# Optimization experiments

Measured on AMD Instinct MI355X. Metric: run time of the kernel, lower is better.

The kernel has to match this reference:

```python
import jax, jax.numpy as jnp
import numpy as np


def setup_inputs() -> dict:
    key = jax.random.key(0)
    k_x, k_pos, k_val, k_temp = jax.random.split(key, 4)
    B, T, D, N = 8, 2048, 512, 4096
    x = jax.random.normal(k_x, (B, T, D), dtype=jnp.float32)
    # module init: positions ~ N(0,1)*0.5, values ~ N(0,1)*0.02
    positions = jax.random.normal(k_pos, (N, D), dtype=jnp.float32) * 0.5
    values = jax.random.normal(k_val, (N, D), dtype=jnp.float32) * 0.02
    # 'trained' temperatures ~ U[4,6] so the RBF kernel does not underflow at D=512
    temperature = 4.0 + 2.0 * jax.random.uniform(k_temp, (N,), dtype=jnp.float32)
    # neuron_scale buffer at late-tide level (MAX_SCALE = 0.8)
    neuron_scale = jnp.full((N,), 0.8, dtype=jnp.float32)
    return {"x": x, "positions": positions, "values": values,
            "temperature": temperature, "neuron_scale": neuron_scale}


def reference(x, positions, values, temperature, neuron_scale):
    B, T, D = x.shape
    x_flat = x.reshape(-1, D)                                  # [M, D], M = B*T
    x_sq = jnp.sum(x_flat * x_flat, axis=-1, keepdims=True)    # [M, 1]
    p_sq = jnp.sum(positions * positions, axis=-1)             # [N]
    cross = x_flat @ positions.T                               # [M, N] GEMM
    dists = jnp.sqrt(jnp.maximum(x_sq + p_sq[None, :] - 2.0 * cross, 0.0))
    effective_temp = (jnp.abs(temperature) + 0.1) * neuron_scale  # [N]
    weights = jnp.exp(-dists / effective_temp[None, :])        # [M, N]
    weights = weights / (jnp.sum(weights, axis=-1, keepdims=True) + 1e-8)
    out = weights @ values                                     # [M, D] GEMM
    return out.reshape(B, T, D)
```

## Files before the change

### kernel.cpp

```cpp
#include <hip/hip_runtime.h>
#include <hip/hip_bf16.h>

typedef __attribute__((ext_vector_type(8))) short short8;
typedef __attribute__((ext_vector_type(4))) float f32x4;
typedef __attribute__((ext_vector_type(4))) unsigned short u16x4;

__device__ __forceinline__ unsigned short f2bf(float f) {
  union { float f; unsigned u; } v; v.f = f;
  unsigned r = v.u + 0x7fffu + ((v.u >> 16) & 1u);
  return (unsigned short)(r >> 16);
}

template <int EPI>
__global__ __launch_bounds__(512, 4) void rbf_gemm(
    const unsigned short* __restrict__ A, const unsigned short* __restrict__ Bt,
    int Ncols, int K,
    const float* __restrict__ xsq, const float* __restrict__ psq,
    const float* __restrict__ rtemp, unsigned short* __restrict__ Wout,
    float* __restrict__ part, int Mtot, const float* __restrict__ denin,
    float* __restrict__ outp, int row0, int ldOut) {
  constexpr int HALF = 16384;
  __shared__ __align__(16) unsigned short smem[2 * HALF];

  const int t = threadIdx.x;
  const int lane = t & 63, wid = t >> 6;
  const int wr = wid >> 1, wc = wid & 1;
  const int lr = lane & 15, lg = lane >> 4;

  const int nb = Ncols >> 7;
  const int nwg = gridDim.x;
  int swz = blockIdx.x;
  if ((nwg & 7) == 0) {
    int cpx = nwg >> 3;
    swz = (swz & 7) * cpx + (swz >> 3);
  }
  const int bm = swz / nb, bn = swz - bm * nb;

  const unsigned short* Ab = A + (size_t)bm * 128 * K;
  const unsigned short* Bb = Bt + (size_t)bn * 128 * K;

  const unsigned short* gA[2];
  const unsigned short* gB[2];
#pragma unroll
  for (int i = 0; i < 2; ++i) {
    const int idx = i * 512 + t;
    const int r = idx >> 3, c = idx & 7;
    const int cs = c ^ (r & 7);
    gA[i] = Ab + (size_t)r * K + cs * 8;
    gB[i] = Bb + (size_t)r * K + cs * 8;
  }
  const int dbase = wid << 9;

  int offA[2][2], offB[4][2];
#pragma unroll
  for (int mi = 0; mi < 2; ++mi) {
    const int ar = wr * 32 + mi * 16 + lr;
#pragma unroll
    for (int ks = 0; ks < 2; ++ks)
      offA[mi][ks] = ar * 64 + (((ks << 2) | lg) ^ (ar & 7)) * 8;
  }
#pragma unroll
  for (int ni = 0; ni < 4; ++ni) {
    const int br = wc * 64 + ni * 16 + lr;
#pragma unroll
    for (int ks = 0; ks < 2; ++ks)
      offB[ni][ks] = 8192 + br * 64 + (((ks << 2) | lg) ^ (br & 7)) * 8;
  }

  f32x4 acc[2][4];
#pragma unroll
  for (int i = 0; i < 2; ++i)
#pragma unroll
    for (int j = 0; j < 4; ++j) acc[i][j] = (f32x4){0.f, 0.f, 0.f, 0.f};

#define STAGE(koff, boff)                                                            \
  do {                                                                               \
    _Pragma("unroll")                                                                \
    for (int i = 0; i < 2; ++i) {                                                    \
      __builtin_amdgcn_global_load_lds(                                              \
          (const __attribute__((address_space(1))) void*)(gA[i] + (koff)),           \
          (__attribute__((address_space(3))) void*)(smem + (boff) + i * 4096 + dbase), \
          16, 0, 0);                                                                 \
      __builtin_amdgcn_global_load_lds(                                              \
          (const __attribute__((address_space(1))) void*)(gB[i] + (koff)),           \
          (__attribute__((address_space(3))) void*)(smem + (boff) + 8192 + i * 4096 + dbase), \
          16, 0, 0);                                                                 \
    }                                                                                \
  } while (0)

  STAGE(0, 0);
  __syncthreads();
  unsigned boff = 0;
  const int nsteps = K >> 6;
  for (int s = 0; s < nsteps; ++s) {
    if (s + 1 < nsteps) STAGE((s + 1) << 6, boff ^ HALF);
    const unsigned short* sb = smem + boff;
    short8 af[2][2], bf[4][2];
#pragma unroll
    for (int mi = 0; mi < 2; ++mi)
#pragma unroll
      for (int ks = 0; ks < 2; ++ks) af[mi][ks] = *(const short8*)&sb[offA[mi][ks]];
#pragma unroll
    for (int ni = 0; ni < 4; ++ni)
#pragma unroll
      for (int ks = 0; ks < 2; ++ks) bf[ni][ks] = *(const short8*)&sb[offB[ni][ks]];
#pragma unroll
    for (int ks = 0; ks < 2; ++ks)
#pragma unroll
      for (int mi = 0; mi < 2; ++mi)
#pragma unroll
        for (int ni = 0; ni < 4; ++ni)
          acc[mi][ni] = __builtin_amdgcn_mfma_f32_16x16x32_bf16(af[mi][ks], bf[ni][ks],
                                                                acc[mi][ni], 0, 0, 0);
    __syncthreads();
    boff ^= HALF;
  }
#undef STAGE

  if (EPI == 0) {
    float xv[2][4];
#pragma unroll
    for (int mi = 0; mi < 2; ++mi)
#pragma unroll
      for (int j = 0; j < 4; ++j)
        xv[mi][j] = xsq[row0 + bm * 128 + wr * 32 + mi * 16 + lg * 4 + j];

    float rs[2][4];
#pragma unroll
    for (int mi = 0; mi < 2; ++mi)
#pragma unroll
      for (int j = 0; j < 4; ++j) rs[mi][j] = 0.f;

#pragma unroll
    for (int ni = 0; ni < 4; ++ni) {
      const int lcol = wc * 64 + ni * 16 + lr;
      const int col = bn * 128 + lcol;
      const float ps = psq[col];
      const float rt = rtemp[col];
      const int h = lcol >> 3;
#pragma unroll
      for (int mi = 0; mi < 2; ++mi) {
#pragma unroll
        for (int j = 0; j < 4; ++j) {
          const int lrow = wr * 32 + mi * 16 + lg * 4 + j;
          float d2 = xv[mi][j] + ps - 2.0f * acc[mi][ni][j];
          float dist = __builtin_amdgcn_sqrtf(fmaxf(d2, 0.0f));
          float wgt = __expf(-dist * rt);
          smem[lrow * 128 + ((h ^ (lrow & 15)) << 3) + (lcol & 7)] = f2bf(wgt);
          rs[mi][j] += wgt;
        }
      }
    }
    __syncthreads();
#pragma unroll
    for (int i = 0; i < 4; ++i) {
      const int id = i * 512 + t;
      const int r = id >> 4, h = id & 15;
      short8 v = *(const short8*)&smem[r * 128 + ((h ^ (r & 15)) << 3)];
      __builtin_nontemporal_store(v,
          (short8*)&Wout[(size_t)(bm * 128 + r) * ldOut + bn * 128 + h * 8]);
    }
    float* slice = part + (size_t)((bn << 1) | wc) * Mtot;
#pragma unroll
    for (int mi = 0; mi < 2; ++mi)
#pragma unroll
      for (int j = 0; j < 4; ++j) {
        float v = rs[mi][j];
        v += __shfl_xor(v, 1);
        v += __shfl_xor(v, 2);
        v += __shfl_xor(v, 4);
        v += __shfl_xor(v, 8);
        if (lr == 0) {
          const int grow = row0 + bm * 128 + wr * 32 + mi * 16 + lg * 4 + j;
          __builtin_nontemporal_store(v, &slice[grow]);
        }
      }
  } else {
#pragma unroll
    for (int mi = 0; mi < 2; ++mi) {
#pragma unroll
      for (int j = 0; j < 4; ++j) {
        const int grow = row0 + bm * 128 + wr * 32 + mi * 16 + lg * 4 + j;
        const float rd = 1.0f / (denin[grow] + 1e-8f);
#pragma unroll
        for (int ni = 0; ni < 4; ++ni) {
          const int col = bn * 128 + wc * 64 + ni * 16 + lr;
          __builtin_nontemporal_store(acc[mi][ni][j] * rd,
                                      &outp[(size_t)grow * ldOut + col]);
        }
      }
    }
  }
}

__global__ void reduce_denom(const float* __restrict__ part, float* __restrict__ denom,
                             int Mtot, int row0, int S) {
  const int m = row0 + blockIdx.x * 128 + threadIdx.x;
  float s = 0.f;
  for (int i = 0; i < S; ++i) s += part[(size_t)i * Mtot + m];
  denom[m] = s;
}

__global__ void prep_rows(const float* __restrict__ in, unsigned short* __restrict__ outb,
                          float* __restrict__ sq, int D) {
  const int row = blockIdx.x;
  const int t = threadIdx.x;
  const float4 v = ((const float4*)(in + (size_t)row * D))[t];
  u16x4 o = {f2bf(v.x), f2bf(v.y), f2bf(v.z), f2bf(v.w)};
  *(u16x4*)(outb + (size_t)row * D + t * 4) = o;
  float s = v.x * v.x + v.y * v.y + v.z * v.z + v.w * v.w;
  for (int off = 32; off; off >>= 1) s += __shfl_xor(s, off);
  __shared__ float ws[16];
  if ((t & 63) == 0) ws[t >> 6] = s;
  __syncthreads();
  if (t == 0) {
    float tot = 0.f;
    const int nw = blockDim.x >> 6;
    for (int i = 0; i < nw; ++i) tot += ws[i];
    sq[row] = tot;
  }
}

__global__ void prep_scale(const float* __restrict__ tmp, const float* __restrict__ sc,
                           float* __restrict__ rtemp, int N) {
  const int i = blockIdx.x * blockDim.x + threadIdx.x;
  if (i < N) rtemp[i] = 1.0f / ((fabsf(tmp[i]) + 0.1f) * sc[i]);
}

__global__ void prep_vT(const float* __restrict__ vals, unsigned short* __restrict__ vT,
                        int N, int D) {
  __shared__ float tile[32][33];
  const int nt = blockIdx.x, dt = blockIdx.y;
  const int tx = threadIdx.x, ty = threadIdx.y;
#pragma unroll
  for (int i = 0; i < 4; ++i) {
    int r = nt * 32 + ty + i * 8;
    tile[ty + i * 8][tx] = vals[(size_t)r * D + dt * 32 + tx];
  }
  __syncthreads();
#pragma unroll
  for (int i = 0; i < 4; ++i) {
    int d = dt * 32 + ty + i * 8;
    vT[(size_t)d * N + nt * 32 + tx] = f2bf(tile[tx][ty + i * 8]);
  }
}

extern "C" void kernel_launch(void* const* d_in, const int* in_sizes, int n_in,
                              void* d_out, int out_size, void* d_ws, size_t ws_size,
                              hipStream_t stream) {
  const float* x = (const float*)d_in[0];
  const float* pos = (const float*)d_in[1];
  const float* vals = (const float*)d_in[2];
  const float* temp = (const float*)d_in[3];
  const float* nsc = (const float*)d_in[4];
  float* out = (float*)d_out;

  const int N = in_sizes[3];
  const int D = in_sizes[1] / N;
  const int M = in_sizes[0] / D;
  const int S = 2 * (N / 128);

  char* ws = (char*)d_ws;
  size_t off = 0;
  auto alloc = [&](size_t bytes) {
    void* p = ws + off;
    off = (off + bytes + 255) & ~(size_t)255;
    return p;
  };
  unsigned short* xb = (unsigned short*)alloc((size_t)M * D * 2);
  unsigned short* pb = (unsigned short*)alloc((size_t)N * D * 2);
  unsigned short* vT = (unsigned short*)alloc((size_t)D * N * 2);
  float* xsq = (float*)alloc((size_t)M * 4);
  float* psq = (float*)alloc((size_t)N * 4);
  float* rtemp = (float*)alloc((size_t)N * 4);
  float* denom = (float*)alloc((size_t)M * 4);
  float* part = (float*)alloc((size_t)S * M * 4);

  size_t avail = ws_size > off ? ws_size - off : 0;
  long long mc_ll = (long long)(avail / ((size_t)N * 2));
  int Mc = (int)((mc_ll / 128) * 128);
  if (Mc > M) Mc = M;
  if (Mc < 128) Mc = 128;
  unsigned short* W = (unsigned short*)alloc((size_t)Mc * N * 2);

  prep_rows<<<M, D / 4, 0, stream>>>(x, xb, xsq, D);
  prep_rows<<<N, D / 4, 0, stream>>>(pos, pb, psq, D);
  prep_scale<<<(N + 255) / 256, 256, 0, stream>>>(temp, nsc, rtemp, N);
  dim3 tg(N / 32, D / 32);
  prep_vT<<<tg, dim3(32, 8), 0, stream>>>(vals, vT, N, D);

  for (int row0 = 0; row0 < M; row0 += Mc) {
    const int mc = (M - row0) < Mc ? (M - row0) : Mc;
    const int g1 = (mc / 128) * (N / 128);
    rbf_gemm<0><<<g1, 512, 0, stream>>>(xb + (size_t)row0 * D, pb, N, D,
                                        xsq, psq, rtemp, W, part, M,
                                        nullptr, nullptr, row0, N);
    reduce_denom<<<mc / 128, 128, 0, stream>>>(part, denom, M, row0, S);
    const int g2 = (mc / 128) * (D / 128);
    rbf_gemm<1><<<g2, 512, 0, stream>>>(W, vT, D, N,
                                        nullptr, nullptr, nullptr, nullptr,
                                        part, M, denom, out, row0, D);
  }
}
```

Before: 230.0 us.

## Fuse distance GEMM, RBF weights and value GEMM into one flash-style kernel

```diff
diff --git a/kernel.cpp b/kernel.cpp
--- a/kernel.cpp
+++ b/kernel.cpp
@@ -11,203 +11,246 @@
   return (unsigned short)(r >> 16);
 }
 
-template <int EPI>
-__global__ __launch_bounds__(512, 4) void rbf_gemm(
-    const unsigned short* __restrict__ A, const unsigned short* __restrict__ Bt,
-    int Ncols, int K,
+#define GLL(src, dst)                                                     \
+  __builtin_amdgcn_global_load_lds(                                       \
+      (const __attribute__((address_space(1))) void*)(src),               \
+      (__attribute__((address_space(3))) void*)(dst), 16, 0, 0)
+#define BAR __builtin_amdgcn_s_barrier()
+
+__global__ __launch_bounds__(512, 2) void rbf_fused(
+    const unsigned short* __restrict__ xb, const unsigned short* __restrict__ pb,
+    const unsigned short* __restrict__ vT,
     const float* __restrict__ xsq, const float* __restrict__ psq,
-    const float* __restrict__ rtemp, unsigned short* __restrict__ Wout,
-    float* __restrict__ part, int Mtot, const float* __restrict__ denin,
-    float* __restrict__ outp, int row0, int ldOut) {
-  constexpr int HALF = 16384;
-  __shared__ __align__(16) unsigned short smem[2 * HALF];
-
+    const float* __restrict__ rtemp, float* __restrict__ out, int N, int Dk) {
+  __shared__ __align__(16) unsigned short smem[65536];
   const int t = threadIdx.x;
   const int lane = t & 63, wid = t >> 6;
-  const int wr = wid >> 1, wc = wid & 1;
   const int lr = lane & 15, lg = lane >> 4;
-
-  const int nb = Ncols >> 7;
-  const int nwg = gridDim.x;
-  int swz = blockIdx.x;
-  if ((nwg & 7) == 0) {
-    int cpx = nwg >> 3;
-    swz = (swz & 7) * cpx + (swz >> 3);
-  }
-  const int bm = swz / nb, bn = swz - bm * nb;
-
-  const unsigned short* Ab = A + (size_t)bm * 128 * K;
-  const unsigned short* Bb = Bt + (size_t)bn * 128 * K;
-
-  const unsigned short* gA[2];
-  const unsigned short* gB[2];
-#pragma unroll
-  for (int i = 0; i < 2; ++i) {
+  const int wm = wid >> 2, wn = wid & 3;
+  const int row0 = blockIdx.x * 64;
+
+  const unsigned short* Xb = xb + (size_t)row0 * Dk;
+
+#pragma unroll
+  for (int i = 0; i < 8; ++i) {
+    const int idx = i * 512 + t;
+    const int r = idx >> 6, c = idx & 63;
+    GLL(Xb + (size_t)r * Dk + ((c ^ (r & 7)) << 3), smem + i * 4096 + (wid << 9));
+  }
+  const unsigned short* gP[4];
+#pragma unroll
+  for (int i = 0; i < 4; ++i) {
     const int idx = i * 512 + t;
     const int r = idx >> 3, c = idx & 7;
-    const int cs = c ^ (r & 7);
-    gA[i] = Ab + (size_t)r * K + cs * 8;
-    gB[i] = Bb + (size_t)r * K + cs * 8;
-  }
-  const int dbase = wid << 9;
-
-  int offA[2][2], offB[4][2];
+    gP[i] = pb + (size_t)r * Dk + ((c ^ (r & 7)) << 3);
+  }
+
+#define STAGE_P(bufb, bump)                                               \
+  do {                                                                    \
+    _Pragma("unroll")                                                     \
+    for (int i = 0; i < 4; ++i) {                                         \
+      GLL(gP[i], smem + 32768 + (bufb) * 16384 + i * 4096 + (wid << 9));  \
+      gP[i] += (bump);                                                    \
+    }                                                                     \
+  } while (0)
+
+  STAGE_P(0, 64);
+
+  int offAx[2][2], offP[4][2], offW[4][2];
 #pragma unroll
   for (int mi = 0; mi < 2; ++mi) {
-    const int ar = wr * 32 + mi * 16 + lr;
+    const int ar = wm * 32 + mi * 16 + lr;
 #pragma unroll
     for (int ks = 0; ks < 2; ++ks)
-      offA[mi][ks] = ar * 64 + (((ks << 2) | lg) ^ (ar & 7)) * 8;
+      offAx[mi][ks] = ar * Dk + ((((ks << 2) | lg) ^ (ar & 7)) << 3);
   }
 #pragma unroll
   for (int ni = 0; ni < 4; ++ni) {
-    const int br = wc * 64 + ni * 16 + lr;
+    const int br = wn * 64 + ni * 16 + lr;
 #pragma unroll
     for (int ks = 0; ks < 2; ++ks)
-      offB[ni][ks] = 8192 + br * 64 + (((ks << 2) | lg) ^ (br & 7)) * 8;
-  }
-
-  f32x4 acc[2][4];
-#pragma unroll
-  for (int i = 0; i < 2; ++i)
-#pragma unroll
-    for (int j = 0; j < 4; ++j) acc[i][j] = (f32x4){0.f, 0.f, 0.f, 0.f};
-
-#define STAGE(koff, boff)                                                            \
-  do {                                                                               \
-    _Pragma("unroll")                                                                \
-    for (int i = 0; i < 2; ++i) {                                                    \
-      __builtin_amdgcn_global_load_lds(                                              \
-          (const __attribute__((address_space(1))) void*)(gA[i] + (koff)),           \
-          (__attribute__((address_space(3))) void*)(smem + (boff) + i * 4096 + dbase), \
-          16, 0, 0);                                                                 \
-      __builtin_amdgcn_global_load_lds(                                              \
-          (const __attribute__((address_space(1))) void*)(gB[i] + (koff)),           \
-          (__attribute__((address_space(3))) void*)(smem + (boff) + 8192 + i * 4096 + dbase), \
-          16, 0, 0);                                                                 \
-    }                                                                                \
-  } while (0)
-
-  STAGE(0, 0);
+      offP[ni][ks] = br * 64 + ((((ks << 2) | lg) ^ (br & 7)) << 3);
+  }
+#pragma unroll
+  for (int mi = 0; mi < 4; ++mi) {
+    const int ar = mi * 16 + lr;
+#pragma unroll
+    for (int ks = 0; ks < 2; ++ks)
+      offW[mi][ks] = 49152 + ar * 256 + ((((ks << 2) | lg) ^ (ar & 7)) << 3);
+  }
+  const unsigned short* vrow[4];
+#pragma unroll
+  for (int ni = 0; ni < 4; ++ni)
+    vrow[ni] = vT + (size_t)(wid * 64 + ni * 16 + lr) * N + lg * 8;
+
+  float xv[2][4];
+#pragma unroll
+  for (int mi = 0; mi < 2; ++mi)
+#pragma unroll
+    for (int j = 0; j < 4; ++j)
+      xv[mi][j] = xsq[row0 + wm * 32 + mi * 16 + lg * 4 + j];
+
+  f32x4 acc2[4][4];
+#pragma unroll
+  for (int i = 0; i < 4; ++i)
+#pragma unroll
+    for (int j = 0; j < 4; ++j) acc2[i][j] = (f32x4){0.f, 0.f, 0.f, 0.f};
+  float dreg[2][4];
+#pragma unroll
+  for (int mi = 0; mi < 2; ++mi)
+#pragma unroll
+    for (int j = 0; j < 4; ++j) dreg[mi][j] = 0.f;
+
+  const int nch = N >> 8;
+  const int nsl = nch * 8;
+  for (int nc = 0; nc < nch; ++nc) {
+    f32x4 acc1[2][4];
+#pragma unroll
+    for (int i = 0; i < 2; ++i)
+#pragma unroll
+      for (int j = 0; j < 4; ++j) acc1[i][j] = (f32x4){0.f, 0.f, 0.f, 0.f};
+    for (int s = 0; s < 8; ++s) {
+      const int ss = nc * 8 + s;
+      if (ss + 1 < nsl) {
+        const int sl = ss + 1;
+        const int bump = 64 + (((sl & 7) == 7) ? 255 * Dk : 0);
+        STAGE_P(sl & 1, bump);
+        asm volatile("s_waitcnt vmcnt(4)" ::: "memory");
+      } else {
+        asm volatile("s_waitcnt vmcnt(0)" ::: "memory");
+      }
+      BAR;
+      const unsigned short* sp = smem + 32768 + (ss & 1) * 16384;
+      const int ko = s * 64;
+      short8 afr[2][2], bfr[4][2];
+#pragma unroll
+      for (int mi = 0; mi < 2; ++mi)
+#pragma unroll
+        for (int ks = 0; ks < 2; ++ks)
+          afr[mi][ks] = *(const short8*)&smem[offAx[mi][ks] + ko];
+#pragma unroll
+      for (int ni = 0; ni < 4; ++ni)
+#pragma unroll
+        for (int ks = 0; ks < 2; ++ks)
+          bfr[ni][ks] = *(const short8*)&sp[offP[ni][ks]];
+      __builtin_amdgcn_s_setprio(1);
+#pragma unroll
+      for (int ks = 0; ks < 2; ++ks)
+#pragma unroll
+        for (int mi = 0; mi < 2; ++mi)
+#pragma unroll
+          for (int ni = 0; ni < 4; ++ni)
+            acc1[mi][ni] = __builtin_amdgcn_mfma_f32_16x16x32_bf16(
+                afr[mi][ks], bfr[ni][ks], acc1[mi][ni], 0, 0, 0);
+      __builtin_amdgcn_s_setprio(0);
+      asm volatile("s_waitcnt lgkmcnt(0)" ::: "memory");
+      BAR;
+    }
+    float ps_[4], rt_[4];
+#pragma unroll
+    for (int ni = 0; ni < 4; ++ni) {
+      const int col = (nc << 8) + wn * 64 + ni * 16 + lr;
+      ps_[ni] = psq[col];
+      rt_[ni] = rtemp[col];
+    }
+#pragma unroll
+    for (int mi = 0; mi < 2; ++mi) {
+#pragma unroll
+      for (int j = 0; j < 4; ++j) {
+        const int lrow = wm * 32 + mi * 16 + lg * 4 + j;
+        float rsv = 0.f;
+#pragma unroll
+        for (int ni = 0; ni < 4; ++ni) {
+          const int lcol = wn * 64 + ni * 16 + lr;
+          float d2 = xv[mi][j] + ps_[ni] - 2.0f * acc1[mi][ni][j];
+          float dist = __builtin_amdgcn_sqrtf(fmaxf(d2, 0.0f));
+          float w = __builtin_amdgcn_exp2f(-dist * rt_[ni]);
+          smem[49152 + lrow * 256 + (((lcol >> 3) ^ (lrow & 7)) << 3) + (lcol & 7)] =
+              f2bf(w);
+          rsv += w;
+        }
+        rsv += __shfl_xor(rsv, 1);
+        rsv += __shfl_xor(rsv, 2);
+        rsv += __shfl_xor(rsv, 4);
+        rsv += __shfl_xor(rsv, 8);
+        dreg[mi][j] += rsv;
+      }
+    }
+    __syncthreads();
+    const int ncoff = nc << 8;
+#pragma unroll
+    for (int s2 = 0; s2 < 4; ++s2) {
+      short8 wfr[4][2], vfr[4][2];
+#pragma unroll
+      for (int mi = 0; mi < 4; ++mi)
+#pragma unroll
+        for (int ks = 0; ks < 2; ++ks)
+          wfr[mi][ks] = *(const short8*)&smem[offW[mi][ks] + s2 * 64];
+#pragma unroll
+      for (int ni = 0; ni < 4; ++ni)
+#pragma unroll
+        for (int ks = 0; ks < 2; ++ks)
+          vfr[ni][ks] = *(const short8*)&vrow[ni][ncoff + s2 * 64 + ks * 32];
+#pragma unroll
+      for (int ks = 0; ks < 2; ++ks)
+#pragma unroll
+        for (int mi = 0; mi < 4; ++mi)
+#pragma unroll
+          for (int ni = 0; ni < 4; ++ni)
+            acc2[mi][ni] = __builtin_amdgcn_mfma_f32_16x16x32_bf16(
+                wfr[mi][ks], vfr[ni][ks], acc2[mi][ni], 0, 0, 0);
+    }
+    __syncthreads();
+  }
+#undef STAGE_P
+
+  float* dsm = (float*)smem;
+  if (lr == 0) {
+#pragma unroll
+    for (int mi = 0; mi < 2; ++mi)
+#pragma unroll
+      for (int j = 0; j < 4; ++j)
+        dsm[wn * 64 + wm * 32 + mi * 16 + lg * 4 + j] = dreg[mi][j];
+  }
   __syncthreads();
-  unsigned boff = 0;
-  const int nsteps = K >> 6;
-  for (int s = 0; s < nsteps; ++s) {
-    if (s + 1 < nsteps) STAGE((s + 1) << 6, boff ^ HALF);
-    const unsigned short* sb = smem + boff;
-    short8 af[2][2], bf[4][2];
-#pragma unroll
-    for (int mi = 0; mi < 2; ++mi)
-#pragma unroll
-      for (int ks = 0; ks < 2; ++ks) af[mi][ks] = *(const short8*)&sb[offA[mi][ks]];
-#pragma unroll
-    for (int ni = 0; ni < 4; ++ni)
-#pragma unroll
-      for (int ks = 0; ks < 2; ++ks) bf[ni][ks] = *(const short8*)&sb[offB[ni][ks]];
-#pragma unroll
-    for (int ks = 0; ks < 2; ++ks)
-#pragma unroll
-      for (int mi = 0; mi < 2; ++mi)
-#pragma unroll
-        for (int ni = 0; ni < 4; ++ni)
-          acc[mi][ni] = __builtin_amdgcn_mfma_f32_16x16x32_bf16(af[mi][ks], bf[ni][ks],
-                                                                acc[mi][ni], 0, 0, 0);
-    __syncthreads();
-    boff ^= HALF;
-  }
-#undef STAGE
-
-  if (EPI == 0) {
-    float xv[2][4];
-#pragma unroll
-    for (int mi = 0; mi < 2; ++mi)
-#pragma unroll
-      for (int j = 0; j < 4; ++j)
-        xv[mi][j] = xsq[row0 + bm * 128 + wr * 32 + mi * 16 + lg * 4 + j];
-
-    float rs[2][4];
-#pragma unroll
-    for (int mi = 0; mi < 2; ++mi)
-#pragma unroll
-      for (int j = 0; j < 4; ++j) rs[mi][j] = 0.f;
-
-#pragma unroll
-    for (int ni = 0; ni < 4; ++ni) {
-      const int lcol = wc * 64 + ni * 16 + lr;
-      const int col = bn * 128 + lcol;
-      const float ps = psq[col];
-      const float rt = rtemp[col];
-      const int h = lcol >> 3;
-#pragma unroll
-      for (int mi = 0; mi < 2; ++mi) {
-#pragma unroll
-        for (int j = 0; j < 4; ++j) {
-          const int lrow = wr * 32 + mi * 16 + lg * 4 + j;
-          float d2 = xv[mi][j] + ps - 2.0f * acc[mi][ni][j];
-          float dist = __builtin_amdgcn_sqrtf(fmaxf(d2, 0.0f));
-          float wgt = __expf(-dist * rt);
-          smem[lrow * 128 + ((h ^ (lrow & 15)) << 3) + (lcol & 7)] = f2bf(wgt);
-          rs[mi][j] += wgt;
-        }
-      }
-    }
-    __syncthreads();
-#pragma unroll
-    for (int i = 0; i < 4; ++i) {
-      const int id = i * 512 + t;
-      const int r = id >> 4, h = id & 15;
-      short8 v = *(const short8*)&smem[r * 128 + ((h ^ (r & 15)) << 3)];
-      __builtin_nontemporal_store(v,
-          (short8*)&Wout[(size_t)(bm * 128 + r) * ldOut + bn * 128 + h * 8]);
-    }
-    float* slice = part + (size_t)((bn << 1) | wc) * Mtot;
-#pragma unroll
-    for (int mi = 0; mi < 2; ++mi)
-#pragma unroll
-      for (int j = 0; j < 4; ++j) {
-        float v = rs[mi][j];
-        v += __shfl_xor(v, 1);
-        v += __shfl_xor(v, 2);
-        v += __shfl_xor(v, 4);
-        v += __shfl_xor(v, 8);
-        if (lr == 0) {
-          const int grow = row0 + bm * 128 + wr * 32 + mi * 16 + lg * 4 + j;
-          __builtin_nontemporal_store(v, &slice[grow]);
-        }
-      }
+  if (t < 64) {
+    float s = dsm[t] + dsm[64 + t] + dsm[128 + t] + dsm[192 + t];
+    dsm[256 + t] = 1.0f / (s + 1e-8f);
+  }
+  __syncthreads();
+#pragma unroll
+  for (int mi = 0; mi < 4; ++mi) {
+#pragma unroll
+    for (int j = 0; j < 4; ++j) {
+      const int row = mi * 16 + lg * 4 + j;
+      const float rd = dsm[256 + row];
+#pragma unroll
+      for (int ni = 0; ni < 4; ++ni)
+        __builtin_nontemporal_store(
+            acc2[mi][ni][j] * rd,
+            &out[(size_t)(row0 + row) * Dk + wid * 64 + ni * 16 + lr]);
+    }
+  }
+}
+
+__global__ void prep_rows2(const float* __restrict__ x, const float* __restrict__ pos,
+                           unsigned short* __restrict__ xb, unsigned short* __restrict__ pb,
+                           float* __restrict__ xsq, float* __restrict__ psq,
+                           int D, int M) {
+  const int row = blockIdx.x;
+  const float* in;
+  unsigned short* outb;
+  float* sq;
+  int r;
+  if (row < M) {
+    in = x; outb = xb; sq = xsq; r = row;
   } else {
-#pragma unroll
-    for (int mi = 0; mi < 2; ++mi) {
-#pragma unroll
-      for (int j = 0; j < 4; ++j) {
-        const int grow = row0 + bm * 128 + wr * 32 + mi * 16 + lg * 4 + j;
-        const float rd = 1.0f / (denin[grow] + 1e-8f);
-#pragma unroll
-        for (int ni = 0; ni < 4; ++ni) {
-          const int col = bn * 128 + wc * 64 + ni * 16 + lr;
-          __builtin_nontemporal_store(acc[mi][ni][j] * rd,
-                                      &outp[(size_t)grow * ldOut + col]);
-        }
-      }
-    }
-  }
-}
-
-__global__ void reduce_denom(const float* __restrict__ part, float* __restrict__ denom,
-                             int Mtot, int row0, int S) {
-  const int m = row0 + blockIdx.x * 128 + threadIdx.x;
-  float s = 0.f;
-  for (int i = 0; i < S; ++i) s += part[(size_t)i * Mtot + m];
-  denom[m] = s;
-}
-
-__global__ void prep_rows(const float* __restrict__ in, unsigned short* __restrict__ outb,
-                          float* __restrict__ sq, int D) {
-  const int row = blockIdx.x;
+    in = pos; outb = pb; sq = psq; r = row - M;
+  }
   const int t = threadIdx.x;
-  const float4 v = ((const float4*)(in + (size_t)row * D))[t];
+  const float4 v = ((const float4*)(in + (size_t)r * D))[t];
   u16x4 o = {f2bf(v.x), f2bf(v.y), f2bf(v.z), f2bf(v.w)};
-  *(u16x4*)(outb + (size_t)row * D + t * 4) = o;
+  *(u16x4*)(outb + (size_t)r * D + t * 4) = o;
   float s = v.x * v.x + v.y * v.y + v.z * v.z + v.w * v.w;
   for (int off = 32; off; off >>= 1) s += __shfl_xor(s, off);
   __shared__ float ws[16];
@@ -217,14 +260,14 @@
     float tot = 0.f;
     const int nw = blockDim.x >> 6;
     for (int i = 0; i < nw; ++i) tot += ws[i];
-    sq[row] = tot;
+    sq[r] = tot;
   }
 }
 
 __global__ void prep_scale(const float* __restrict__ tmp, const float* __restrict__ sc,
                            float* __restrict__ rtemp, int N) {
   const int i = blockIdx.x * blockDim.x + threadIdx.x;
-  if (i < N) rtemp[i] = 1.0f / ((fabsf(tmp[i]) + 0.1f) * sc[i]);
+  if (i < N) rtemp[i] = 1.4426950408889634f / ((fabsf(tmp[i]) + 0.1f) * sc[i]);
 }
 
 __global__ void prep_vT(const float* __restrict__ vals, unsigned short* __restrict__ vT,
@@ -258,7 +301,6 @@
   const int N = in_sizes[3];
   const int D = in_sizes[1] / N;
   const int M = in_sizes[0] / D;
-  const int S = 2 * (N / 128);
 
   char* ws = (char*)d_ws;
   size_t off = 0;
@@ -273,32 +315,11 @@
   float* xsq = (float*)alloc((size_t)M * 4);
   float* psq = (float*)alloc((size_t)N * 4);
   float* rtemp = (float*)alloc((size_t)N * 4);
-  float* denom = (float*)alloc((size_t)M * 4);
-  float* part = (float*)alloc((size_t)S * M * 4);
-
-  size_t avail = ws_size > off ? ws_size - off : 0;
-  long long mc_ll = (long long)(avail / ((size_t)N * 2));
-  int Mc = (int)((mc_ll / 128) * 128);
-  if (Mc > M) Mc = M;
-  if (Mc < 128) Mc = 128;
-  unsigned short* W = (unsigned short*)alloc((size_t)Mc * N * 2);
-
-  prep_rows<<<M, D / 4, 0, stream>>>(x, xb, xsq, D);
-  prep_rows<<<N, D / 4, 0, stream>>>(pos, pb, psq, D);
+
+  prep_rows2<<<M + N, D / 4, 0, stream>>>(x, pos, xb, pb, xsq, psq, D, M);
   prep_scale<<<(N + 255) / 256, 256, 0, stream>>>(temp, nsc, rtemp, N);
   dim3 tg(N / 32, D / 32);
   prep_vT<<<tg, dim3(32, 8), 0, stream>>>(vals, vT, N, D);
 
-  for (int row0 = 0; row0 < M; row0 += Mc) {
-    const int mc = (M - row0) < Mc ? (M - row0) : Mc;
-    const int g1 = (mc / 128) * (N / 128);
-    rbf_gemm<0><<<g1, 512, 0, stream>>>(xb + (size_t)row0 * D, pb, N, D,
-                                        xsq, psq, rtemp, W, part, M,
-                                        nullptr, nullptr, row0, N);
-    reduce_denom<<<mc / 128, 128, 0, stream>>>(part, denom, M, row0, S);
-    const int g2 = (mc / 128) * (D / 128);
-    rbf_gemm<1><<<g2, 512, 0, stream>>>(W, vT, D, N,
-                                        nullptr, nullptr, nullptr, nullptr,
-                                        part, M, denom, out, row0, D);
-  }
-}
+  rbf_fused<<<M / 64, 512, 0, stream>>>(xb, pb, vT, xsq, psq, rtemp, out, N, D);
+}
```

Result: slower. 256.4 us (+11.5%).
